# Kernel tuning notes

Measured on AMD Instinct MI355X. Metric: run time of the kernel, lower is better.

The kernel has to match this reference:

```python
import jax, jax.numpy as jnp
import numpy as np

N, E, IN_DIM, HID, OUT = 50000, 800000, 128, 64, 64


def setup_inputs() -> dict:
    key = jax.random.key(0)
    ks = jax.random.split(key, 8)
    x = jax.random.normal(ks[0], (N, IN_DIM), dtype=jnp.float32)
    edge_index = jax.random.randint(ks[1], (2, E), 0, N, dtype=jnp.int64)
    # Glorot-style init like PyG GCNConv linear; bias zeros-init equivalent -> small randn for generality
    def glorot(k, fan_in, fan_out):
        s = (6.0 / (fan_in + fan_out)) ** 0.5
        return jax.random.uniform(k, (fan_in, fan_out), jnp.float32, -s, s)
    W1 = glorot(ks[2], IN_DIM, HID)
    b1 = jnp.zeros((HID,), jnp.float32)
    W2 = glorot(ks[3], HID, HID)
    b2 = jnp.zeros((HID,), jnp.float32)
    W3 = glorot(ks[4], HID, OUT)
    b3 = jnpp = jnp.zeros((OUT,), jnp.float32)
    return {"x": x, "edge_index": edge_index, "W1": W1, "b1": b1,
            "W2": W2, "b2": b2, "W3": W3, "b3": b3}


def _gcn_norm(edge_index, num_nodes):
    # PyG gcn_norm with add_self_loops=True, edge_weight=1:
    # A_hat = A + I; deg over target column; norm = d^-1/2[src] * d^-1/2[dst]
    loops = jnp.arange(num_nodes, dtype=edge_index.dtype)
    src = jnp.concatenate([edge_index[0], loops])
    dst = jnp.concatenate([edge_index[1], loops])
    ones = jnp.ones(src.shape[0], dtype=jnp.float32)
    deg = jax.ops.segment_sum(ones, dst, num_segments=num_nodes)
    dinv = jnp.where(deg > 0, jax.lax.rsqrt(deg), 0.0)
    norm = dinv[src] * dinv[dst]  # [E+N]
    return src, dst, norm


def _conv(h, src, dst, norm, W, b, num_nodes):
    h = h @ W                         # [N, F_out] dense transform first (PyG order)
    msg = norm[:, None] * h[src]      # gather + degree-normalize, [E+N, F_out]
    out = jax.ops.segment_sum(msg, dst, num_segments=num_nodes)  # scatter-add
    return out + b


def reference(x, edge_index, W1, b1, W2, b2, W3, b3):
    num_nodes = x.shape[0]
    src, dst, norm = _gcn_norm(edge_index, num_nodes)
    h = _conv(x, src, dst, norm, W1, b1, num_nodes)
    h = jax.nn.relu(h)  # dropout is identity in eval / p=0
    h = _conv(h, src, dst, norm, W2, b2, num_nodes)
    h = jax.nn.relu(h)
    h = _conv(h, src, dst, norm, W3, b3, num_nodes)
    return h
```

## Files before the change

### kernel.cpp

```cpp
#include <hip/hip_runtime.h>


#define FD 64
#define P1CHUNK 4096

typedef unsigned short ushort_t;
typedef unsigned int uint_t;

__device__ __forceinline__ ushort_t f2bf(float f) {
    uint_t u = __float_as_uint(f);
    u = (u + 0x7fffu + ((u >> 16) & 1u)) >> 16;
    return (ushort_t)u;
}
__device__ __forceinline__ uint_t pack2bf(float f0, float f1) {
    return (uint_t)f2bf(f0) | ((uint_t)f2bf(f1) << 16);
}

__global__ __launch_bounds__(256) void bucket_count(const int* __restrict__ dst,
                                                    int* __restrict__ bucketCnt, int E) {
    __shared__ int hist[256];
    int tid = threadIdx.x;
    hist[tid] = 0;
    __syncthreads();
    int base = blockIdx.x * P1CHUNK;
#pragma unroll
    for (int k = 0; k < 16; ++k) {
        int e = base + k * 256 + tid;
        if (e < E) atomicAdd(&hist[dst[e] >> 8], 1);
    }
    __syncthreads();
    int h = hist[tid];
    if (h) atomicAdd(&bucketCnt[tid], h);
}

__global__ __launch_bounds__(256) void scan_buckets(const int* __restrict__ bucketCnt,
                                                    int* __restrict__ bucketBase,
                                                    int* __restrict__ bucketCursor,
                                                    int* __restrict__ rowptr,
                                                    int NB, int N, int E) {
    __shared__ int wsum[4];
    int tid = threadIdx.x, lane = tid & 63, wv = tid >> 6;
    int v = (tid < NB) ? bucketCnt[tid] : 0;
    int x = v;
    for (int off = 1; off < 64; off <<= 1) {
        int t = __shfl_up(x, off, 64);
        if (lane >= off) x += t;
    }
    if (lane == 63) wsum[wv] = x;
    __syncthreads();
    int wex = 0;
    for (int i = 0; i < wv; ++i) wex += wsum[i];
    int excl = wex + x - v;
    if (tid < NB) { bucketBase[tid] = excl; bucketCursor[tid] = excl; }
    if (tid == 0) { bucketBase[NB] = E; rowptr[N] = E; }
}

template <int K, bool SCALE>
__device__ __forceinline__ void gemm_body(int bid, const float* __restrict__ x,
                                          const float* __restrict__ W,
                                          const float* __restrict__ dinv,
                                          ushort_t* __restrict__ out, int nrows,
                                          float* Xs ) {
    constexpr int KP = K + 4;
    constexpr int NC = K / 4;
    constexpr int YP = 68;
    const int tid = threadIdx.x;
    const int lane = tid & 63;
    const int rowBase = bid * 64;

    for (int idx = tid; idx < 64 * NC; idx += 256) {
        int row = idx / NC, kc = idx % NC;
        int r = rowBase + row;
        float4 v = (r < nrows) ? *(const float4*)(x + (size_t)r * K + kc * 4)
                               : make_float4(0.f, 0.f, 0.f, 0.f);
        *(float4*)(&Xs[row * KP + kc * 4]) = v;
    }
    __syncthreads();

    const int c0 = __builtin_amdgcn_readfirstlane((tid >> 6) * 16);
    float acc[16];
#pragma unroll
    for (int i = 0; i < 16; ++i) acc[i] = 0.f;
    const float* Xrow = &Xs[lane * KP];

#pragma unroll 4
    for (int k = 0; k < K; k += 4) {
        float4 xv = *(const float4*)(Xrow + k);
        const float* wp = W + (size_t)k * FD + c0;
#pragma unroll
        for (int ci = 0; ci < 16; ++ci) {
            acc[ci] = fmaf(xv.x, wp[ci], acc[ci]);
            acc[ci] = fmaf(xv.y, wp[FD + ci], acc[ci]);
            acc[ci] = fmaf(xv.z, wp[2 * FD + ci], acc[ci]);
            acc[ci] = fmaf(xv.w, wp[3 * FD + ci], acc[ci]);
        }
    }

    int r = rowBase + lane;
    float di = 1.0f;
    if (SCALE) di = (r < nrows) ? dinv[r] : 0.f;
    __syncthreads();
    float* Ys = Xs;
#pragma unroll
    for (int ci = 0; ci < 16; ++ci) Ys[lane * YP + c0 + ci] = acc[ci] * di;
    __syncthreads();

    for (int i = tid; i < 64 * 16; i += 256) {
        int row = i >> 4, seg = i & 15;
        int rr = rowBase + row;
        if (rr < nrows) {
            float4 v = *(const float4*)(&Ys[row * YP + seg * 4]);
            uint2 p;
            p.x = pack2bf(v.x, v.y);
            p.y = pack2bf(v.z, v.w);
            *(uint2*)(out + (size_t)rr * FD + seg * 4) = p;
        }
    }
}

template <int K>
__global__ __launch_bounds__(256) void gemm_kernel(const float* __restrict__ x,
                                                   const float* __restrict__ W,
                                                   const float* __restrict__ dinv,
                                                   ushort_t* __restrict__ out, int nrows) {
    __shared__ float Xs[64 * (K + 4)];
    gemm_body<K, true>(blockIdx.x, x, W, dinv, out, nrows, Xs);
}

__global__ __launch_bounds__(256) void fused_gemm1_scatter(
    const float* __restrict__ x, const float* __restrict__ W1,
    ushort_t* __restrict__ hB, int nrows,
    const int* __restrict__ src, const int* __restrict__ dst,
    int* __restrict__ bucketCursor, uint_t* __restrict__ staged, int E,
    int nGemmBlk) {
    __shared__ float Xs[64 * 132];
    int bid = blockIdx.x;
    if (bid < nGemmBlk) {
        gemm_body<128, false>(bid, x, W1, nullptr, hB, nrows, Xs);
        return;
    }
    int* hist = (int*)Xs;
    int* gbase = hist + 256;
    int tid = threadIdx.x;
    hist[tid] = 0;
    __syncthreads();
    int base = (bid - nGemmBlk) * P1CHUNK;
#pragma unroll
    for (int k = 0; k < 16; ++k) {
        int e = base + k * 256 + tid;
        if (e < E) atomicAdd(&hist[dst[e] >> 8], 1);
    }
    __syncthreads();
    int h = hist[tid];
    gbase[tid] = h ? atomicAdd(&bucketCursor[tid], h) : 0;
    hist[tid] = 0;
    __syncthreads();
#pragma unroll
    for (int k = 0; k < 16; ++k) {
        int e = base + k * 256 + tid;
        if (e < E) {
            int s = src[e], d = dst[e];
            int b = d >> 8;
            int r = atomicAdd(&hist[b], 1);
            staged[gbase[b] + r] = (uint_t)s | ((uint_t)(d & 255) << 16);
        }
    }
}

__global__ __launch_bounds__(256) void bucket_sort(const uint_t* __restrict__ staged,
                                                   const int* __restrict__ bucketBase,
                                                   int* __restrict__ rowptr,
                                                   float* __restrict__ dinv,
                                                   ushort_t* __restrict__ csr,
                                                   ushort_t* __restrict__ hB, int N) {
    __shared__ int ncnt[256];
    __shared__ int nrp[256];
    __shared__ int wsum[4];
    __shared__ float sdinv[256];
    int tid = threadIdx.x, lane = tid & 63, wv = tid >> 6;
    int b = blockIdx.x;
    int gbeg = bucketBase[b], gend = bucketBase[b + 1];
    int cntE = gend - gbeg;
    ncnt[tid] = 0;
    __syncthreads();
    for (int i = tid; i < cntE; i += 256)
        atomicAdd(&ncnt[(staged[gbeg + i] >> 16) & 255], 1);
    __syncthreads();
    int v = ncnt[tid];
    int x = v;
    for (int off = 1; off < 64; off <<= 1) {
        int t = __shfl_up(x, off, 64);
        if (lane >= off) x += t;
    }
    if (lane == 63) wsum[wv] = x;
    __syncthreads();
    int wex = 0;
    for (int i = 0; i < wv; ++i) wex += wsum[i];
    int excl = wex + x - v;
    nrp[tid] = excl;
    int node = b * 256 + tid;
    float di = rsqrtf((float)(v + 1));
    sdinv[tid] = di;
    if (node < N) dinv[node] = di;
    if (node <= N) rowptr[node] = gbeg + excl;
    ncnt[tid] = 0;
    __syncthreads();
    for (int i = tid; i < cntE; i += 256) {
        uint_t p = staged[gbeg + i];
        int dl = (p >> 16) & 255;
        int lofs = atomicAdd(&ncnt[dl], 1);
        csr[(size_t)gbeg + nrp[dl] + lofs] = (ushort_t)(p & 0xffffu);
    }
    uint2* hB2 = (uint2*)hB;
    for (int idx = tid; idx < 256 * 16; idx += 256) {
        int row = idx >> 4, c = idx & 15;
        int g = b * 256 + row;
        if (g < N) {
            float d = sdinv[row];
            uint2 u = hB2[(size_t)g * 16 + c];
            float f0 = __uint_as_float(u.x << 16) * d;
            float f1 = __uint_as_float(u.x & 0xffff0000u) * d;
            float f2 = __uint_as_float(u.y << 16) * d;
            float f3 = __uint_as_float(u.y & 0xffff0000u) * d;
            uint2 o;
            o.x = pack2bf(f0, f1);
            o.y = pack2bf(f2, f3);
            hB2[(size_t)g * 16 + c] = o;
        }
    }
}

__device__ __forceinline__ void bf8_acc(uint4 a, float* acc) {
    acc[0] += __uint_as_float(a.x << 16);
    acc[1] += __uint_as_float(a.x & 0xffff0000u);
    acc[2] += __uint_as_float(a.y << 16);
    acc[3] += __uint_as_float(a.y & 0xffff0000u);
    acc[4] += __uint_as_float(a.z << 16);
    acc[5] += __uint_as_float(a.z & 0xffff0000u);
    acc[6] += __uint_as_float(a.w << 16);
    acc[7] += __uint_as_float(a.w & 0xffff0000u);
}

template <bool RELU>
__global__ __launch_bounds__(256) void agg_fused(
    const int* __restrict__ rowptr, const ushort_t* __restrict__ csr,
    const float* __restrict__ dinv, const ushort_t* __restrict__ h,
    const float* __restrict__ b, float* __restrict__ out, int N) {
    int wid = (blockIdx.x * blockDim.x + threadIdx.x) >> 6;
    int lane = threadIdx.x & 63;
    int l8 = lane & 7;
    int node = wid * 8 + (lane >> 3);
    bool valid = node < N;
    int nd = valid ? node : N - 1;
    int beg = rowptr[nd];
    int end = valid ? rowptr[nd + 1] : beg;
    const uint4* __restrict__ h4 = (const uint4*)h;
    float acc[8];
#pragma unroll
    for (int k = 0; k < 8; ++k) acc[k] = 0.f;
    bf8_acc(h4[(size_t)nd * 8 + l8], acc);
    int j = beg;
    for (; j + 3 < end; j += 4) {
        int s0 = csr[j], s1 = csr[j + 1], s2 = csr[j + 2], s3 = csr[j + 3];
        uint4 a0 = h4[(size_t)s0 * 8 + l8];
        uint4 a1 = h4[(size_t)s1 * 8 + l8];
        uint4 a2 = h4[(size_t)s2 * 8 + l8];
        uint4 a3 = h4[(size_t)s3 * 8 + l8];
        bf8_acc(a0, acc); bf8_acc(a1, acc); bf8_acc(a2, acc); bf8_acc(a3, acc);
    }
    for (; j < end; ++j) bf8_acc(h4[(size_t)csr[j] * 8 + l8], acc);

    float di = dinv[nd];
    float4 b0 = *(const float4*)(b + l8 * 8);
    float4 b1 = *(const float4*)(b + l8 * 8 + 4);
    float4 v0, v1;
    v0.x = fmaf(di, acc[0], b0.x); v0.y = fmaf(di, acc[1], b0.y);
    v0.z = fmaf(di, acc[2], b0.z); v0.w = fmaf(di, acc[3], b0.w);
    v1.x = fmaf(di, acc[4], b1.x); v1.y = fmaf(di, acc[5], b1.y);
    v1.z = fmaf(di, acc[6], b1.z); v1.w = fmaf(di, acc[7], b1.w);
    if (RELU) {
        v0.x = fmaxf(v0.x, 0.f); v0.y = fmaxf(v0.y, 0.f);
        v0.z = fmaxf(v0.z, 0.f); v0.w = fmaxf(v0.w, 0.f);
        v1.x = fmaxf(v1.x, 0.f); v1.y = fmaxf(v1.y, 0.f);
        v1.z = fmaxf(v1.z, 0.f); v1.w = fmaxf(v1.w, 0.f);
    }
    if (valid) {
        float* op = out + (size_t)node * FD + l8 * 8;
        *(float4*)op = v0;
        *(float4*)(op + 4) = v1;
    }
}

extern "C" void kernel_launch(void* const* d_in, const int* in_sizes, int n_in,
                              void* d_out, int out_size, void* d_ws, size_t ws_size,
                              hipStream_t stream) {
    const float* x  = (const float*)d_in[0];
    const int*   ei = (const int*)d_in[1];
    const float* W1 = (const float*)d_in[2];
    const float* b1 = (const float*)d_in[3];
    const float* W2 = (const float*)d_in[4];
    const float* b2 = (const float*)d_in[5];
    const float* W3 = (const float*)d_in[6];
    const float* b3 = (const float*)d_in[7];
    float* out = (float*)d_out;

    const int N = in_sizes[0] / 128;
    const int E = in_sizes[1] / 2;
    const int* src = ei;
    const int* dst = ei + E;
    const int NB = (N + 255) / 256;

    float*    f1     = (float*)d_ws;
    ushort_t* hB     = (ushort_t*)(f1 + (size_t)N * FD);
    float*    dinv   = (float*)(hB + (size_t)N * FD);
    int*      rowptr = (int*)(dinv + N);
    int*   bucketCnt    = rowptr + N + 1;
    int*   bucketBase   = bucketCnt + NB;
    int*   bucketCursor = bucketBase + NB + 1;
    uint_t*   staged = (uint_t*)(bucketCursor + NB);
    ushort_t* csr    = (ushort_t*)(staged + E);

    const int nSctBlk = (E + P1CHUNK - 1) / P1CHUNK;
    const int nGemmBlk = (N + 63) / 64;
    dim3 blk(256);
    dim3 gGemm(nGemmBlk);
    dim3 gAgg((N + 31) / 32);

    hipMemsetAsync(bucketCnt, 0, (size_t)NB * sizeof(int), stream);
    bucket_count<<<dim3(nSctBlk), blk, 0, stream>>>(dst, bucketCnt, E);
    scan_buckets<<<dim3(1), blk, 0, stream>>>(bucketCnt, bucketBase, bucketCursor,
                                              rowptr, NB, N, E);
    fused_gemm1_scatter<<<dim3(nGemmBlk + nSctBlk), blk, 0, stream>>>(
        x, W1, hB, N, src, dst, bucketCursor, staged, E, nGemmBlk);
    bucket_sort<<<dim3(NB), blk, 0, stream>>>(staged, bucketBase, rowptr, dinv,
                                              csr, hB, N);

    agg_fused<true><<<gAgg, blk, 0, stream>>>(rowptr, csr, dinv, hB, b1, f1, N);

    gemm_kernel<64><<<gGemm, blk, 0, stream>>>(f1, W2, dinv, hB, N);
    agg_fused<true><<<gAgg, blk, 0, stream>>>(rowptr, csr, dinv, hB, b2, f1, N);

    gemm_kernel<64><<<gGemm, blk, 0, stream>>>(f1, W3, dinv, hB, N);
    agg_fused<false><<<gAgg, blk, 0, stream>>>(rowptr, csr, dinv, hB, b3, out, N);
}
```

Baseline: 143.1 us.

## Drop bucket count pass with fixed-capacity buckets; sort nodes by degree for aggregation

```diff
diff --git a/kernel.cpp b/kernel.cpp
--- a/kernel.cpp
+++ b/kernel.cpp
@@ -3,6 +3,7 @@
 
 #define FD 64
 #define P1CHUNK 4096
+#define CAP 8192
 
 typedef unsigned short ushort_t;
 typedef unsigned int uint_t;
@@ -16,31 +17,13 @@
     return (uint_t)f2bf(f0) | ((uint_t)f2bf(f1) << 16);
 }
 
-__global__ __launch_bounds__(256) void bucket_count(const int* __restrict__ dst,
-                                                    int* __restrict__ bucketCnt, int E) {
-    __shared__ int hist[256];
-    int tid = threadIdx.x;
-    hist[tid] = 0;
-    __syncthreads();
-    int base = blockIdx.x * P1CHUNK;
-#pragma unroll
-    for (int k = 0; k < 16; ++k) {
-        int e = base + k * 256 + tid;
-        if (e < E) atomicAdd(&hist[dst[e] >> 8], 1);
-    }
-    __syncthreads();
-    int h = hist[tid];
-    if (h) atomicAdd(&bucketCnt[tid], h);
-}
-
-__global__ __launch_bounds__(256) void scan_buckets(const int* __restrict__ bucketCnt,
+__global__ __launch_bounds__(256) void scan_buckets(const int* __restrict__ cnt,
                                                     int* __restrict__ bucketBase,
-                                                    int* __restrict__ bucketCursor,
                                                     int* __restrict__ rowptr,
                                                     int NB, int N, int E) {
     __shared__ int wsum[4];
     int tid = threadIdx.x, lane = tid & 63, wv = tid >> 6;
-    int v = (tid < NB) ? bucketCnt[tid] : 0;
+    int v = (tid < NB) ? min(cnt[tid], CAP) : 0;
     int x = v;
     for (int off = 1; off < 64; off <<= 1) {
         int t = __shfl_up(x, off, 64);
@@ -51,7 +34,7 @@
     int wex = 0;
     for (int i = 0; i < wv; ++i) wex += wsum[i];
     int excl = wex + x - v;
-    if (tid < NB) { bucketBase[tid] = excl; bucketCursor[tid] = excl; }
+    if (tid < NB) bucketBase[tid] = excl;
     if (tid == 0) { bucketBase[NB] = E; rowptr[N] = E; }
 }
 
@@ -131,8 +114,7 @@
     const float* __restrict__ x, const float* __restrict__ W1,
     ushort_t* __restrict__ hB, int nrows,
     const int* __restrict__ src, const int* __restrict__ dst,
-    int* __restrict__ bucketCursor, uint_t* __restrict__ staged, int E,
-    int nGemmBlk) {
+    int* __restrict__ cnt, uint_t* __restrict__ staged, int E, int nGemmBlk) {
     __shared__ float Xs[64 * 132];
     int bid = blockIdx.x;
     if (bid < nGemmBlk) {
@@ -152,7 +134,7 @@
     }
     __syncthreads();
     int h = hist[tid];
-    gbase[tid] = h ? atomicAdd(&bucketCursor[tid], h) : 0;
+    gbase[tid] = h ? atomicAdd(&cnt[tid], h) : 0;
     hist[tid] = 0;
     __syncthreads();
 #pragma unroll
@@ -162,29 +144,35 @@
             int s = src[e], d = dst[e];
             int b = d >> 8;
             int r = atomicAdd(&hist[b], 1);
-            staged[gbase[b] + r] = (uint_t)s | ((uint_t)(d & 255) << 16);
+            int p = gbase[b] + r;
+            if (p < CAP) staged[(size_t)b * CAP + p] = (uint_t)s | ((uint_t)(d & 255) << 16);
         }
     }
 }
 
 __global__ __launch_bounds__(256) void bucket_sort(const uint_t* __restrict__ staged,
+                                                   const int* __restrict__ cnt,
                                                    const int* __restrict__ bucketBase,
                                                    int* __restrict__ rowptr,
                                                    float* __restrict__ dinv,
                                                    ushort_t* __restrict__ csr,
-                                                   ushort_t* __restrict__ hB, int N) {
+                                                   ushort_t* __restrict__ hB,
+                                                   int* __restrict__ dhist, int N) {
     __shared__ int ncnt[256];
     __shared__ int nrp[256];
     __shared__ int wsum[4];
     __shared__ float sdinv[256];
+    __shared__ int dh[64];
     int tid = threadIdx.x, lane = tid & 63, wv = tid >> 6;
     int b = blockIdx.x;
-    int gbeg = bucketBase[b], gend = bucketBase[b + 1];
-    int cntE = gend - gbeg;
+    int gbeg = bucketBase[b];
+    int cntE = min(cnt[b], CAP);
+    const uint_t* sb = staged + (size_t)b * CAP;
     ncnt[tid] = 0;
+    if (tid < 64) dh[tid] = 0;
     __syncthreads();
     for (int i = tid; i < cntE; i += 256)
-        atomicAdd(&ncnt[(staged[gbeg + i] >> 16) & 255], 1);
+        atomicAdd(&ncnt[(sb[i] >> 16) & 255], 1);
     __syncthreads();
     int v = ncnt[tid];
     int x = v;
@@ -201,12 +189,16 @@
     int node = b * 256 + tid;
     float di = rsqrtf((float)(v + 1));
     sdinv[tid] = di;
-    if (node < N) dinv[node] = di;
+    if (node < N) {
+        dinv[node] = di;
+        atomicAdd(&dh[min(v, 63)], 1);
+    }
     if (node <= N) rowptr[node] = gbeg + excl;
     ncnt[tid] = 0;
     __syncthreads();
+    if (tid < 64 && dh[tid]) atomicAdd(&dhist[tid], dh[tid]);
     for (int i = tid; i < cntE; i += 256) {
-        uint_t p = staged[gbeg + i];
+        uint_t p = sb[i];
         int dl = (p >> 16) & 255;
         int lofs = atomicAdd(&ncnt[dl], 1);
         csr[(size_t)gbeg + nrp[dl] + lofs] = (ushort_t)(p & 0xffffu);
@@ -230,6 +222,45 @@
     }
 }
 
+__global__ void deg_scan(const int* __restrict__ dhist, int* __restrict__ dcursor) {
+    int lane = threadIdx.x;
+    int v = dhist[lane];
+    int x = v;
+    for (int off = 1; off < 64; off <<= 1) {
+        int t = __shfl_up(x, off, 64);
+        if (lane >= off) x += t;
+    }
+    dcursor[lane] = x - v;
+}
+
+__global__ __launch_bounds__(256) void deg_scatter(const int* __restrict__ rowptr,
+                                                   int* __restrict__ dcursor,
+                                                   int* __restrict__ perm, int N) {
+    __shared__ int h[64];
+    __shared__ int gb[64];
+    int tid = threadIdx.x;
+    if (tid < 64) h[tid] = 0;
+    __syncthreads();
+    int node = blockIdx.x * 256 + tid;
+    bool val = node < N;
+    int d = 0;
+    if (val) {
+        d = min(rowptr[node + 1] - rowptr[node], 63);
+        atomicAdd(&h[d], 1);
+    }
+    __syncthreads();
+    if (tid < 64) {
+        int c = h[tid];
+        gb[tid] = c ? atomicAdd(&dcursor[tid], c) : 0;
+        h[tid] = 0;
+    }
+    __syncthreads();
+    if (val) {
+        int r = atomicAdd(&h[d], 1);
+        perm[gb[d] + r] = node;
+    }
+}
+
 __device__ __forceinline__ void bf8_acc(uint4 a, float* acc) {
     acc[0] += __uint_as_float(a.x << 16);
     acc[1] += __uint_as_float(a.x & 0xffff0000u);
@@ -244,14 +275,15 @@
 template <bool RELU>
 __global__ __launch_bounds__(256) void agg_fused(
     const int* __restrict__ rowptr, const ushort_t* __restrict__ csr,
+    const int* __restrict__ perm,
     const float* __restrict__ dinv, const ushort_t* __restrict__ h,
     const float* __restrict__ b, float* __restrict__ out, int N) {
     int wid = (blockIdx.x * blockDim.x + threadIdx.x) >> 6;
     int lane = threadIdx.x & 63;
     int l8 = lane & 7;
-    int node = wid * 8 + (lane >> 3);
-    bool valid = node < N;
-    int nd = valid ? node : N - 1;
+    int widx = wid * 8 + (lane >> 3);
+    bool valid = widx < N;
+    int nd = perm[valid ? widx : 0];
     int beg = rowptr[nd];
     int end = valid ? rowptr[nd + 1] : beg;
     const uint4* __restrict__ h4 = (const uint4*)h;
@@ -285,7 +317,7 @@
         v1.z = fmaxf(v1.z, 0.f); v1.w = fmaxf(v1.w, 0.f);
     }
     if (valid) {
-        float* op = out + (size_t)node * FD + l8 * 8;
+        float* op = out + (size_t)nd * FD + l8 * 8;
         *(float4*)op = v0;
         *(float4*)(op + 4) = v1;
     }
@@ -314,11 +346,13 @@
     ushort_t* hB     = (ushort_t*)(f1 + (size_t)N * FD);
     float*    dinv   = (float*)(hB + (size_t)N * FD);
     int*      rowptr = (int*)(dinv + N);
-    int*   bucketCnt    = rowptr + N + 1;
-    int*   bucketBase   = bucketCnt + NB;
-    int*   bucketCursor = bucketBase + NB + 1;
-    uint_t*   staged = (uint_t*)(bucketCursor + NB);
-    ushort_t* csr    = (ushort_t*)(staged + E);
+    int*   cnt       = rowptr + N + 1;
+    int*   dhist     = cnt + NB;
+    int*   dcursor   = dhist + 64;
+    int*   bucketBase= dcursor + 64;
+    int*   perm      = bucketBase + NB + 1;
+    uint_t*   staged = (uint_t*)(perm + N);
+    ushort_t* csr    = (ushort_t*)(staged + (size_t)NB * CAP);
 
     const int nSctBlk = (E + P1CHUNK - 1) / P1CHUNK;
     const int nGemmBlk = (N + 63) / 64;
@@ -326,20 +360,20 @@
     dim3 gGemm(nGemmBlk);
     dim3 gAgg((N + 31) / 32);
 
-    hipMemsetAsync(bucketCnt, 0, (size_t)NB * sizeof(int), stream);
-    bucket_count<<<dim3(nSctBlk), blk, 0, stream>>>(dst, bucketCnt, E);
-    scan_buckets<<<dim3(1), blk, 0, stream>>>(bucketCnt, bucketBase, bucketCursor,
-                                              rowptr, NB, N, E);
+    hipMemsetAsync(cnt, 0, (size_t)(NB + 64) * sizeof(int), stream);
     fused_gemm1_scatter<<<dim3(nGemmBlk + nSctBlk), blk, 0, stream>>>(
-        x, W1, hB, N, src, dst, bucketCursor, staged, E, nGemmBlk);
-    bucket_sort<<<dim3(NB), blk, 0, stream>>>(staged, bucketBase, rowptr, dinv,
-                                              csr, hB, N);
-
-    agg_fused<true><<<gAgg, blk, 0, stream>>>(rowptr, csr, dinv, hB, b1, f1, N);
+        x, W1, hB, N, src, dst, cnt, staged, E, nGemmBlk);
+    scan_buckets<<<dim3(1), blk, 0, stream>>>(cnt, bucketBase, rowptr, NB, N, E);
+    bucket_sort<<<dim3(NB), blk, 0, stream>>>(staged, cnt, bucketBase, rowptr, dinv,
+                                              csr, hB, dhist, N);
+    deg_scan<<<dim3(1), dim3(64), 0, stream>>>(dhist, dcursor);
+    deg_scatter<<<dim3(NB), blk, 0, stream>>>(rowptr, dcursor, perm, N);
+
+    agg_fused<true><<<gAgg, blk, 0, stream>>>(rowptr, csr, perm, dinv, hB, b1, f1, N);
 
     gemm_kernel<64><<<gGemm, blk, 0, stream>>>(f1, W2, dinv, hB, N);
-    agg_fused<true><<<gAgg, blk, 0, stream>>>(rowptr, csr, dinv, hB, b2, f1, N);
+    agg_fused<true><<<gAgg, blk, 0, stream>>>(rowptr, csr, perm, dinv, hB, b2, f1, N);
 
     gemm_kernel<64><<<gGemm, blk, 0, stream>>>(f1, W3, dinv, hB, N);
-    agg_fused<false><<<gAgg, blk, 0, stream>>>(rowptr, csr, dinv, hB, b3, out, N);
-}
+    agg_fused<false><<<gAgg, blk, 0, stream>>>(rowptr, csr, perm, dinv, hB, b3, out, N);
+}
```

Result: no change. 141.1 us (-1.4%).
